# Performance work log

Hardware: AMD Instinct MI355X
Metric: run time of the kernel (lower is better)

## Reference

```python
import jax, jax.numpy as jnp
import numpy as np

B, L, D_IN, H = 16, 2048, 1024, 512  # bidirectional: out_size = 2*H = D_IN (k=3 SRU layout)


def setup_inputs() -> dict:
    key = jax.random.key(0)
    k1, k2, k3, k4 = jax.random.split(key, 4)
    x = jax.random.normal(k1, (B, L, D_IN), dtype=jnp.float32)
    W = jax.random.normal(k2, (D_IN, 2, H, 3), dtype=jnp.float32) * 0.02
    bf = jax.random.normal(k3, (2, H), dtype=jnp.float32) * 0.02
    br = jax.random.normal(k4, (2, H), dtype=jnp.float32) * 0.02
    return {"x": x, "W": W, "bf": bf, "br": br}


def _sru_scan(xtil, f, r, xres, reverse):
    # xtil/f/r/xres: (L, B, H). Diagonal linear recurrence:
    #   c_t = f_t * c_{t-1} + (1 - f_t) * xtil_t
    #   h_t = r_t * tanh(c_t) + (1 - r_t) * xres_t
    def step(c, inp):
        xt_, f_, r_, xr_ = inp
        c = f_ * c + (1.0 - f_) * xt_
        h = r_ * jnp.tanh(c) + (1.0 - r_) * xr_
        return c, h
    c0 = jnp.zeros(xtil.shape[1:], dtype=xtil.dtype)
    c_last, h = jax.lax.scan(step, c0, (xtil, f, r, xres), reverse=reverse)
    return h, c_last


def reference(x, W, bf, br):
    xt = jnp.transpose(x, (1, 0, 2))  # (L, B, D_IN), as the wrapper does x.transpose(0,1)
    # U: (L, B, 2 dirs, H, 3 = [x_tilde, f_pre, r_pre])
    U = jnp.einsum("lbi,idhk->lbdhk", xt, W)
    f = jax.nn.sigmoid(U[..., 1] + bf[None, None, :, :])  # (L,B,2,H)
    r = jax.nn.sigmoid(U[..., 2] + br[None, None, :, :])
    xtil = U[..., 0]
    # highway/residual: raw input split per direction since n_in == 2*H (k=3)
    xres = xt.reshape(L, B, 2, H)

    h_f, c_f = _sru_scan(xtil[:, :, 0], f[:, :, 0], r[:, :, 0], xres[:, :, 0], reverse=False)
    h_b, c_b = _sru_scan(xtil[:, :, 1], f[:, :, 1], r[:, :, 1], xres[:, :, 1], reverse=True)

    h = jnp.concatenate([h_f, h_b], axis=-1)          # (L, B, 2H)
    c = jnp.concatenate([c_f, c_b], axis=-1)          # (B, 2H) final cell states
    # wrapper returns (out.transpose(0,1), c.transpose(0,1))
    return jnp.transpose(h, (1, 0, 2)), c.T
```

## Files before the change

### kernel.cpp

```cpp
#include <hip/hip_runtime.h>
#include <stdint.h>

#define B_    16
#define L_    2048
#define DIN_  1024
#define H_    512
#define NCOL_ 3072
#define M_    (B_ * L_)
#define K_    DIN_
#define NCHUNK 16
#define CHUNK  128

typedef unsigned short u16;
typedef __bf16 bf16_t;
typedef bf16_t bf16x8 __attribute__((ext_vector_type(8)));
typedef float  f32x4  __attribute__((ext_vector_type(4)));

__device__ __forceinline__ u16 f2bf(float f) {
  union { float f; uint32_t u; } v; v.f = f;
  return (u16)((v.u + 0x7fffu + ((v.u >> 16) & 1u)) >> 16);
}
__device__ __forceinline__ float bf2f(u16 b) {
  union { uint32_t u; float f; } v; v.u = ((uint32_t)b) << 16; return v.f;
}
__device__ __forceinline__ u16 f2h(float f) {
  _Float16 h = (_Float16)f; return *(u16*)&h;
}
__device__ __forceinline__ float h2f(u16 b) {
  _Float16 h = *(_Float16*)&b; return (float)h;
}

__global__ void cvt_x_kernel(const float4* __restrict__ x, ushort4* __restrict__ xb) {
  int i = blockIdx.x * blockDim.x + threadIdx.x;
  float4 v = x[i];
  ushort4 o;
  o.x = f2bf(v.x); o.y = f2bf(v.y); o.z = f2bf(v.z); o.w = f2bf(v.w);
  xb[i] = o;
}

__global__ void transpose_w_kernel(const float* __restrict__ W, u16* __restrict__ Wt) {
  __shared__ float s[32][33];
  int n0 = blockIdx.x * 32;
  int i0 = blockIdx.y * 32;
  int tx = threadIdx.x, ty = threadIdx.y;
  #pragma unroll
  for (int y = 0; y < 32; y += 8)
    s[ty + y][tx] = W[(uint64_t)(i0 + ty + y) * NCOL_ + n0 + tx];
  __syncthreads();
  #pragma unroll
  for (int y = 0; y < 32; y += 8) {
    int n = n0 + ty + y;
    int kk = n % 3, d = n / 1536, h = (n % 1536) / 3;
    int np = kk * 1024 + d * 512 + h;
    Wt[(uint64_t)np * K_ + i0 + tx] = f2bf(s[tx][ty + y]);
  }
}

__device__ __forceinline__ void gload_lds16(const void* g, void* lds) {
  __builtin_amdgcn_global_load_lds(
      (const __attribute__((address_space(1))) uint32_t*)g,
      (__attribute__((address_space(3))) uint32_t*)lds, 16, 0, 0);
}

__device__ __forceinline__ bf16x8 lds_rd(const u16* lds, int byteOff) {
  return __builtin_bit_cast(bf16x8, *(const f32x4*)((const char*)lds + byteOff));
}

__global__ __launch_bounds__(512, 2) void gemm_u_kernel(const u16* __restrict__ A,
                                                        const u16* __restrict__ Bt,
                                                        const float* __restrict__ bfp,
                                                        const float* __restrict__ brp,
                                                        u16* __restrict__ xtilP,
                                                        u16* __restrict__ fP,
                                                        u16* __restrict__ rP) {
  __shared__ __align__(16) u16 lds[65536];

  const int bid = blockIdx.x;
  const int xcd = bid & 7;
  const int li  = bid >> 3;
  const int bm  = xcd * 16 + (li & 15);
  const int bn  = li >> 4;
  const int m0 = bm * 256, n0 = bn * 256;

  const int tid  = threadIdx.x;
  const int w    = tid >> 6, lane = tid & 63;
  const int wr   = w >> 2, wc = w & 3;
  const int rr   = lane & 15, hs = lane >> 4;
  const int swzRd = (rr & 7) << 4;
  const int hsOff = hs * 16;

  const int rStage = w * 8 + (lane >> 3);
  const int sCol   = ((lane & 7) ^ ((lane >> 3) & 7)) * 8;
  const int ldsChunk = w * 1024;

  f32x4 acc[8][4] = {};

  auto stageA = [&](int bufBase, int kt) {
    #pragma unroll
    for (int h = 0; h < 2; ++h)
      #pragma unroll
      for (int j = 0; j < 2; ++j)
        gload_lds16(A + (uint64_t)(m0 + h * 128 + j * 64 + rStage) * K_ + kt + sCol,
                    (char*)lds + bufBase + h * 16384 + j * 8192 + ldsChunk);
  };
  auto stageB = [&](int bufBase, int kt) {
    #pragma unroll
    for (int h = 0; h < 2; ++h)
      #pragma unroll
      for (int j = 0; j < 2; ++j)
        gload_lds16(Bt + (uint64_t)(n0 + h * 128 + j * 64 + rStage) * K_ + kt + sCol,
                    (char*)lds + bufBase + 32768 + h * 16384 + j * 8192 + ldsChunk);
  };

  stageA(0, 0); stageB(0, 0);
  asm volatile("s_waitcnt vmcnt(0)" ::: "memory");
  __builtin_amdgcn_s_barrier();

  const int aHalfBase = wr * 16384;
  const int bHalfBase = 32768 + (wc >> 1) * 16384;
  const int rowB0 = (wc & 1) * 64;

  for (int t = 0; t < 16; ++t) {
    const int curBase = (t & 1) * 65536;
    const int nxtBase = curBase ^ 65536;
    const bool pf = (t < 15);
    const int ktNext = (t + 1) * 64;

    bf16x8 bF[4][2];
    #pragma unroll
    for (int q = 0; q < 4; ++q) {
      bf16x8 aF[2][2];
      #pragma unroll
      for (int m2 = 0; m2 < 2; ++m2) {
        const int rowA = (q * 2 + m2) * 16 + rr;
        #pragma unroll
        for (int ks = 0; ks < 2; ++ks)
          aF[m2][ks] = lds_rd(lds, curBase + aHalfBase + rowA * 128 + ((ks * 64 + hsOff) ^ swzRd));
      }
      if (q == 0) {
        #pragma unroll
        for (int ni = 0; ni < 4; ++ni) {
          const int rowB = rowB0 + ni * 16 + rr;
          #pragma unroll
          for (int ks = 0; ks < 2; ++ks)
            bF[ni][ks] = lds_rd(lds, curBase + bHalfBase + rowB * 128 + ((ks * 64 + hsOff) ^ swzRd));
        }
        if (pf) stageA(nxtBase, ktNext);
      }
      if (q == 1 && pf) stageB(nxtBase, ktNext);

      __builtin_amdgcn_sched_barrier(0);
      __builtin_amdgcn_s_barrier();
      asm volatile("s_waitcnt lgkmcnt(0)" ::: "memory");
      __builtin_amdgcn_sched_barrier(0);
      __builtin_amdgcn_s_setprio(1);
      #pragma unroll
      for (int m2 = 0; m2 < 2; ++m2)
        #pragma unroll
        for (int ni = 0; ni < 4; ++ni)
          #pragma unroll
          for (int ks = 0; ks < 2; ++ks)
            acc[q * 2 + m2][ni] = __builtin_amdgcn_mfma_f32_16x16x32_bf16(
                aF[m2][ks], bF[ni][ks], acc[q * 2 + m2][ni], 0, 0, 0);
      __builtin_amdgcn_s_setprio(0);
      if (q == 3 && pf) {
        asm volatile("s_waitcnt vmcnt(0)" ::: "memory");
        __builtin_amdgcn_sched_barrier(0);
      }
      __builtin_amdgcn_s_barrier();
    }
  }

  const int kkPlane = n0 >> 10;
  const int chBase  = n0 & 1023;
  u16* plane = (kkPlane == 0) ? xtilP : (kkPlane == 1 ? fP : rP);
  const float* biasp = (kkPlane == 1) ? bfp : brp;
  #pragma unroll
  for (int mi = 0; mi < 8; ++mi) {
    #pragma unroll
    for (int ni = 0; ni < 4; ++ni) {
      const int ch = chBase + wc * 64 + ni * 16 + rr;
      const float bias = kkPlane ? biasp[ch] : 0.f;
      #pragma unroll
      for (int i = 0; i < 4; ++i) {
        const int row = m0 + wr * 128 + mi * 16 + hs * 4 + i;
        float v = acc[mi][ni][i];
        if (kkPlane) v = 1.f / (1.f + __expf(-(v + bias)));
        plane[(uint64_t)row * 1024 + ch] = f2h(v);
      }
    }
  }
}

__global__ __launch_bounds__(256) void scan_partial_kernel(const u16* __restrict__ xtilP,
                                                           const u16* __restrict__ fP,
                                                           float* __restrict__ cpart,
                                                           float* __restrict__ Pp) {
  int tid = blockIdx.x * 256 + threadIdx.x;
  int ch = tid & 1023, chunk = (tid >> 10) & (NCHUNK - 1), b = tid >> 14;
  int d = ch >> 9;
  int l = chunk * CHUNK + (d ? CHUNK - 1 : 0);
  int64_t stride = d ? -1024 : 1024;
  uint64_t base = ((uint64_t)b * L_ + l) * 1024 + ch;
  float c = 0.f, P = 1.f;
  #pragma unroll 4
  for (int it = 0; it < CHUNK; ++it) {
    float f  = h2f(fP[base]);
    float xt = h2f(xtilP[base]);
    c = f * c + (1.f - f) * xt;
    P *= f;
    base += stride;
  }
  int o = (b * NCHUNK + chunk) * 1024 + ch;
  cpart[o] = c;
  Pp[o] = P;
}

__global__ void scan_combine_kernel(const float* __restrict__ cpart, const float* __restrict__ Pp,
                                    float* __restrict__ cin, float* __restrict__ outc) {
  int tid = blockIdx.x * blockDim.x + threadIdx.x;
  int ch = tid & 1023, b = tid >> 10, d = ch >> 9;
  float c = 0.f;
  for (int i = 0; i < NCHUNK; ++i) {
    int chunk = d ? (NCHUNK - 1 - i) : i;
    int o = (b * NCHUNK + chunk) * 1024 + ch;
    cin[o] = c;
    c = cpart[o] + Pp[o] * c;
  }
  outc[ch * B_ + b] = c;
}

__global__ __launch_bounds__(256) void scan_final_kernel(const u16* __restrict__ xb,
                                                         const u16* __restrict__ xtilP,
                                                         const u16* __restrict__ fP,
                                                         const u16* __restrict__ rP,
                                                         const float* __restrict__ cin,
                                                         float* __restrict__ outh) {
  int tid = blockIdx.x * 256 + threadIdx.x;
  int ch = tid & 1023, chunk = (tid >> 10) & (NCHUNK - 1), b = tid >> 14;
  int d = ch >> 9;
  int l = chunk * CHUNK + (d ? CHUNK - 1 : 0);
  int64_t stride = d ? -1024 : 1024;
  uint64_t base = ((uint64_t)b * L_ + l) * 1024 + ch;
  float c = cin[(b * NCHUNK + chunk) * 1024 + ch];
  #pragma unroll 2
  for (int it = 0; it < CHUNK; ++it) {
    float f    = h2f(fP[base]);
    float xt   = h2f(xtilP[base]);
    float rr   = h2f(rP[base]);
    float xres = bf2f(xb[base]);
    c = f * c + (1.f - f) * xt;
    float th = 1.f - 2.f / (__expf(2.f * c) + 1.f);
    outh[base] = rr * th + (1.f - rr) * xres;
    base += stride;
  }
}

extern "C" void kernel_launch(void* const* d_in, const int* in_sizes, int n_in,
                              void* d_out, int out_size, void* d_ws, size_t ws_size,
                              hipStream_t stream) {
  const float* x   = (const float*)d_in[0];
  const float* W   = (const float*)d_in[1];
  const float* bfp = (const float*)d_in[2];
  const float* brp = (const float*)d_in[3];

  float* outh = (float*)d_out;
  float* outc = outh + (size_t)B_ * L_ * DIN_;

  u16* xb = (u16*)d_ws;
  u16* Wt = xb + (size_t)M_ * K_;
  u16* xtilP = Wt + (size_t)NCOL_ * K_;
  u16* fP    = xtilP + (size_t)M_ * 1024;
  u16* rP    = fP    + (size_t)M_ * 1024;
  float* cpart = (float*)Wt;
  float* Pp    = cpart + (size_t)B_ * NCHUNK * 1024;
  float* cin   = Pp    + (size_t)B_ * NCHUNK * 1024;

  cvt_x_kernel<<<(M_ * K_ / 4) / 256, 256, 0, stream>>>((const float4*)x, (ushort4*)xb);
  transpose_w_kernel<<<dim3(NCOL_ / 32, K_ / 32), dim3(32, 8), 0, stream>>>(W, Wt);
  gemm_u_kernel<<<(M_ / 256) * (NCOL_ / 256), 512, 0, stream>>>(xb, Wt, bfp, brp, xtilP, fP, rP);
  scan_partial_kernel<<<(B_ * NCHUNK * 1024) / 256, 256, 0, stream>>>(xtilP, fP, cpart, Pp);
  scan_combine_kernel<<<(B_ * 2 * H_) / 256, 256, 0, stream>>>(cpart, Pp, cin, outc);
  scan_final_kernel<<<(B_ * NCHUNK * 1024) / 256, 256, 0, stream>>>(xb, xtilP, fP, rP, cin, outh);
}
```

Before: 386.2 us.

## Triple-buffer B tiles and halve barriers in GEMM main loop

The GEMM main loop is restructured so A tiles are double-buffered and B tiles are triple-buffered, with B prefetched two k-tiles ahead. The four quarter-steps per k-tile become two halves, which cuts the number of workgroup barriers per tile. Each half loads four A fragments and runs a larger batch of MFMAs. The aim is to hide global-to-LDS latency and reduce synchronisation stalls. The cost is raising LDS use from 128 KB to 160 KB per block and holding more fragment registers live at once.

```diff
diff --git a/kernel.cpp b/kernel.cpp
--- a/kernel.cpp
+++ b/kernel.cpp
@@ -73,7 +73,7 @@
                                                         u16* __restrict__ xtilP,
                                                         u16* __restrict__ fP,
                                                         u16* __restrict__ rP) {
-  __shared__ __align__(16) u16 lds[65536];
+  __shared__ __align__(16) u16 lds[81920];
 
   const int bid = blockIdx.x;
   const int xcd = bid & 7;
@@ -109,66 +109,84 @@
       #pragma unroll
       for (int j = 0; j < 2; ++j)
         gload_lds16(Bt + (uint64_t)(n0 + h * 128 + j * 64 + rStage) * K_ + kt + sCol,
-                    (char*)lds + bufBase + 32768 + h * 16384 + j * 8192 + ldsChunk);
+                    (char*)lds + bufBase + h * 16384 + j * 8192 + ldsChunk);
   };
 
-  stageA(0, 0); stageB(0, 0);
-  asm volatile("s_waitcnt vmcnt(0)" ::: "memory");
+  stageA(0, 0);
+  stageB(65536, 0);
+  stageB(65536 + 32768, 64);
+  asm volatile("s_waitcnt vmcnt(4)" ::: "memory");
+  __builtin_amdgcn_sched_barrier(0);
   __builtin_amdgcn_s_barrier();
 
   const int aHalfBase = wr * 16384;
-  const int bHalfBase = 32768 + (wc >> 1) * 16384;
-  const int rowB0 = (wc & 1) * 64;
-
+  const int bQuart    = (wc >> 1) * 16384;
+  const int rowB0     = (wc & 1) * 64;
+
+  int b3 = 0;
   for (int t = 0; t < 16; ++t) {
-    const int curBase = (t & 1) * 65536;
-    const int nxtBase = curBase ^ 65536;
-    const bool pf = (t < 15);
-    const int ktNext = (t + 1) * 64;
-
-    bf16x8 bF[4][2];
-    #pragma unroll
-    for (int q = 0; q < 4; ++q) {
-      bf16x8 aF[2][2];
-      #pragma unroll
-      for (int m2 = 0; m2 < 2; ++m2) {
-        const int rowA = (q * 2 + m2) * 16 + rr;
+    const int curA = (t & 1) << 15;
+    const int curB = 65536 + b3 * 32768;
+    const int b3n2 = (b3 >= 1) ? (b3 - 1) : 2;
+
+    if (t < 15) stageA((~t & 1) << 15, (t + 1) * 64);
+    bf16x8 aF[4][2], bF[4][2];
+    #pragma unroll
+    for (int a = 0; a < 4; ++a)
+      #pragma unroll
+      for (int ks = 0; ks < 2; ++ks)
+        aF[a][ks] = lds_rd(lds, curA + aHalfBase + (a * 16 + rr) * 128 + ((ks * 64 + hsOff) ^ swzRd));
+    #pragma unroll
+    for (int ni = 0; ni < 4; ++ni)
+      #pragma unroll
+      for (int ks = 0; ks < 2; ++ks)
+        bF[ni][ks] = lds_rd(lds, curB + bQuart + (rowB0 + ni * 16 + rr) * 128 + ((ks * 64 + hsOff) ^ swzRd));
+    __builtin_amdgcn_sched_barrier(0);
+    __builtin_amdgcn_s_barrier();
+    asm volatile("s_waitcnt lgkmcnt(0)" ::: "memory");
+    __builtin_amdgcn_sched_barrier(0);
+    __builtin_amdgcn_s_setprio(1);
+    #pragma unroll
+    for (int a = 0; a < 4; ++a)
+      #pragma unroll
+      for (int ni = 0; ni < 4; ++ni)
         #pragma unroll
         for (int ks = 0; ks < 2; ++ks)
-          aF[m2][ks] = lds_rd(lds, curBase + aHalfBase + rowA * 128 + ((ks * 64 + hsOff) ^ swzRd));
-      }
-      if (q == 0) {
+          acc[a][ni] = __builtin_amdgcn_mfma_f32_16x16x32_bf16(aF[a][ks], bF[ni][ks], acc[a][ni], 0, 0, 0);
+    __builtin_amdgcn_s_setprio(0);
+    __builtin_amdgcn_sched_barrier(0);
+    __builtin_amdgcn_s_barrier();
+
+    if (t < 14) stageB(65536 + b3n2 * 32768, (t + 2) * 64);
+    bf16x8 aG[4][2];
+    #pragma unroll
+    for (int a = 0; a < 4; ++a)
+      #pragma unroll
+      for (int ks = 0; ks < 2; ++ks)
+        aG[a][ks] = lds_rd(lds, curA + aHalfBase + ((a + 4) * 16 + rr) * 128 + ((ks * 64 + hsOff) ^ swzRd));
+    __builtin_amdgcn_sched_barrier(0);
+    __builtin_amdgcn_s_barrier();
+    asm volatile("s_waitcnt lgkmcnt(0)" ::: "memory");
+    __builtin_amdgcn_sched_barrier(0);
+    __builtin_amdgcn_s_setprio(1);
+    #pragma unroll
+    for (int a = 0; a < 4; ++a)
+      #pragma unroll
+      for (int ni = 0; ni < 4; ++ni)
         #pragma unroll
-        for (int ni = 0; ni < 4; ++ni) {
-          const int rowB = rowB0 + ni * 16 + rr;
-          #pragma unroll
-          for (int ks = 0; ks < 2; ++ks)
-            bF[ni][ks] = lds_rd(lds, curBase + bHalfBase + rowB * 128 + ((ks * 64 + hsOff) ^ swzRd));
-        }
-        if (pf) stageA(nxtBase, ktNext);
-      }
-      if (q == 1 && pf) stageB(nxtBase, ktNext);
-
+        for (int ks = 0; ks < 2; ++ks)
+          acc[a + 4][ni] = __builtin_amdgcn_mfma_f32_16x16x32_bf16(aG[a][ks], bF[ni][ks], acc[a + 4][ni], 0, 0, 0);
+    __builtin_amdgcn_s_setprio(0);
+    if (t < 14) {
+      asm volatile("s_waitcnt vmcnt(4)" ::: "memory");
       __builtin_amdgcn_sched_barrier(0);
-      __builtin_amdgcn_s_barrier();
-      asm volatile("s_waitcnt lgkmcnt(0)" ::: "memory");
+    } else if (t == 14) {
+      asm volatile("s_waitcnt vmcnt(0)" ::: "memory");
       __builtin_amdgcn_sched_barrier(0);
-      __builtin_amdgcn_s_setprio(1);
-      #pragma unroll
-      for (int m2 = 0; m2 < 2; ++m2)
-        #pragma unroll
-        for (int ni = 0; ni < 4; ++ni)
-          #pragma unroll
-          for (int ks = 0; ks < 2; ++ks)
-            acc[q * 2 + m2][ni] = __builtin_amdgcn_mfma_f32_16x16x32_bf16(
-                aF[m2][ks], bF[ni][ks], acc[q * 2 + m2][ni], 0, 0, 0);
-      __builtin_amdgcn_s_setprio(0);
-      if (q == 3 && pf) {
-        asm volatile("s_waitcnt vmcnt(0)" ::: "memory");
-        __builtin_amdgcn_sched_barrier(0);
-      }
-      __builtin_amdgcn_s_barrier();
     }
+    __builtin_amdgcn_s_barrier();
+
+    b3 = (b3 + 1 == 3) ? 0 : b3 + 1;
   }
 
   const int kkPlane = n0 >> 10;
```

Result: no change. 384.6 us (-0.4%).
